# Optimization experiments

Hardware: AMD Instinct MI355X
Metric: run time of the kernel (lower is better)

The kernel has to match this reference:

```python
import jax, jax.numpy as jnp
import numpy as np


def setup_inputs() -> dict:
    key = jax.random.key(0)
    k1, k2 = jax.random.split(key)
    # [1, D, H, W, C] cubic feature volume
    image_features = jax.random.normal(k1, (1, 64, 64, 64, 64), dtype=jnp.float32)
    # [1, N, 3] vertex coords in the original 128^3 volume, in [0, 128)
    graph_features = jax.random.uniform(k2, (1, 200000, 3), dtype=jnp.float32) * 128.0
    return {"image_features": image_features, "graph_features": graph_features}


def reference(image_features, graph_features):
    img = image_features[0]                      # [D, H, W, C]
    H = img.shape[0]
    factor = jnp.float32(128.0 / H)
    x = graph_features[..., -3] / factor         # [B, N]
    y = graph_features[..., -2] / factor
    z = graph_features[..., -1] / factor
    hm1 = jnp.float32(H - 1)
    x1 = jnp.floor(x); x2 = jnp.minimum(jnp.ceil(x), hm1)
    y1 = jnp.floor(y); y2 = jnp.minimum(jnp.ceil(y), hm1)
    z1 = jnp.floor(z); z2 = jnp.minimum(jnp.ceil(z), hm1)

    def gather(ix, iy, iz):
        # [B, N] index arrays -> [B, N, C] gathered features
        return img[ix.astype(jnp.int32), iy.astype(jnp.int32), iz.astype(jnp.int32)]

    wx = (x - x1)[..., None]; wx2 = (x2 - x)[..., None]
    wy = (y - y1)[..., None]; wy2 = (y2 - y)[..., None]
    wz = (z - z1)[..., None]; wz2 = (z2 - z)[..., None]

    # z = z1 plane
    q11 = gather(x1, y1, z1); q21 = gather(x2, y1, z1)
    q12 = gather(x1, y2, z1); q22 = gather(x2, y2, z1)
    lerp_y1 = (q22 * wx + q12 * wx2) * wy + (q21 * wx + q11 * wx2) * wy2

    # z = z2 plane
    q11 = gather(x1, y1, z2); q21 = gather(x2, y1, z2)
    q12 = gather(x1, y2, z2); q22 = gather(x2, y2, z2)
    lerp_y2 = (q22 * wx + q12 * wx2) * wy + (q21 * wx + q11 * wx2) * wy2

    return lerp_y2 * wz + lerp_y1 * wz2          # [B, N, C]
```

## Files before the change

### kernel.cpp

```cpp
#include <hip/hip_runtime.h>


__device__ __forceinline__ float4 f4mul(float4 a, float s) {
    return make_float4(a.x * s, a.y * s, a.z * s, a.w * s);
}
__device__ __forceinline__ float4 f4fma(float4 a, float s, float4 acc) {
    return make_float4(fmaf(a.x, s, acc.x), fmaf(a.y, s, acc.y),
                       fmaf(a.z, s, acc.z), fmaf(a.w, s, acc.w));
}

__global__ __launch_bounds__(256) void trilerp_kernel(
    const float* __restrict__ img, const float* __restrict__ coords,
    float* __restrict__ out, int n_points)
{
    int tid = blockIdx.x * 256 + threadIdx.x;
    int p = tid >> 4;
    if (p >= n_points) return;
    int cvec = tid & 15;

    float x = coords[3 * p + 0] * 0.5f;
    float y = coords[3 * p + 1] * 0.5f;
    float z = coords[3 * p + 2] * 0.5f;

    float fx1 = floorf(x), fx2 = fminf(ceilf(x), 63.0f);
    float fy1 = floorf(y), fy2 = fminf(ceilf(y), 63.0f);
    float fz1 = floorf(z), fz2 = fminf(ceilf(z), 63.0f);

    float wx = x - fx1, wxc = fx2 - x;
    float wy = y - fy1, wyc = fy2 - y;
    float wz = z - fz1, wzc = fz2 - z;

    int ix1 = (int)fx1, ix2 = (int)fx2;
    int iy1 = (int)fy1, iy2 = (int)fy2;
    int iz1 = (int)fz1, iz2 = (int)fz2;

    const float4* __restrict__ imgv = (const float4*)img;
    int bx1 = ix1 << 12, bx2 = ix2 << 12;
    int by1 = iy1 << 6,  by2 = iy2 << 6;

    float4 q11 = imgv[((bx1 + by1 + iz1) << 4) + cvec];
    float4 q21 = imgv[((bx2 + by1 + iz1) << 4) + cvec];
    float4 q12 = imgv[((bx1 + by2 + iz1) << 4) + cvec];
    float4 q22 = imgv[((bx2 + by2 + iz1) << 4) + cvec];
    float4 ly1 = f4fma(f4fma(q22, wx, f4mul(q12, wxc)), wy,
                       f4mul(f4fma(q21, wx, f4mul(q11, wxc)), wyc));

    q11 = imgv[((bx1 + by1 + iz2) << 4) + cvec];
    q21 = imgv[((bx2 + by1 + iz2) << 4) + cvec];
    q12 = imgv[((bx1 + by2 + iz2) << 4) + cvec];
    q22 = imgv[((bx2 + by2 + iz2) << 4) + cvec];
    float4 ly2 = f4fma(f4fma(q22, wx, f4mul(q12, wxc)), wy,
                       f4mul(f4fma(q21, wx, f4mul(q11, wxc)), wyc));

    float4 res = f4fma(ly2, wz, f4mul(ly1, wzc));
    ((float4*)out)[(p << 4) + cvec] = res;
}

extern "C" void kernel_launch(void* const* d_in, const int* in_sizes, int n_in,
                              void* d_out, int out_size, void* d_ws, size_t ws_size,
                              hipStream_t stream) {
    const float* img    = (const float*)d_in[0];
    const float* coords = (const float*)d_in[1];
    float* out = (float*)d_out;
    int n_points = in_sizes[1] / 3;

    int threads = n_points * 16;
    int grid = (threads + 255) / 256;
    trilerp_kernel<<<grid, 256, 0, stream>>>(img, coords, out, n_points);
}
```

Before: 147.7 us.

## Sort points by Morton bin before trilinear gather for cache locality

Adds a counting sort of the points into 32768 Morton-ordered spatial bins (histogram, single-block scan, atomic scatter into a workspace buffer). The gather kernel then walks points in sorted order, so nearby points share cached voxel neighborhoods, and it remaps block IDs so each XCD handles a contiguous range of bins. The aim is to cut the random 16 MB volume gathers that miss in L2. The cost is four extra launches plus a memset, a serial single-block scan, and scattered output writes indexed by the original point ID.

```diff
diff --git a/kernel.cpp b/kernel.cpp
--- a/kernel.cpp
+++ b/kernel.cpp
@@ -1,5 +1,9 @@
 #include <hip/hip_runtime.h>
 
+
+#define NBINS 32768
+#define SCAN_THREADS 1024
+#define BINS_PER_THREAD 32
 
 __device__ __forceinline__ float4 f4mul(float4 a, float s) {
     return make_float4(a.x * s, a.y * s, a.z * s, a.w * s);
@@ -7,6 +11,118 @@
 __device__ __forceinline__ float4 f4fma(float4 a, float s, float4 acc) {
     return make_float4(fmaf(a.x, s, acc.x), fmaf(a.y, s, acc.y),
                        fmaf(a.z, s, acc.z), fmaf(a.w, s, acc.w));
+}
+
+__device__ __forceinline__ unsigned part1by2(unsigned x) {
+    x &= 0x3FF;
+    x = (x | (x << 16)) & 0x030000FF;
+    x = (x | (x << 8))  & 0x0300F00F;
+    x = (x | (x << 4))  & 0x030C30C3;
+    x = (x | (x << 2))  & 0x09249249;
+    return x;
+}
+
+__device__ __forceinline__ int bin_of(float xs, float ys, float zs) {
+    unsigned bx = ((unsigned)(int)floorf(xs)) >> 1;
+    unsigned by = ((unsigned)(int)floorf(ys)) >> 1;
+    unsigned bz = ((unsigned)(int)floorf(zs)) >> 1;
+    return (int)(part1by2(bx) | (part1by2(by) << 1) | (part1by2(bz) << 2));
+}
+
+__global__ __launch_bounds__(256) void hist_kernel(
+    const float* __restrict__ coords, int* __restrict__ bins, int n)
+{
+    int p = blockIdx.x * 256 + threadIdx.x;
+    if (p >= n) return;
+    float xs = coords[3 * p + 0] * 0.5f;
+    float ys = coords[3 * p + 1] * 0.5f;
+    float zs = coords[3 * p + 2] * 0.5f;
+    atomicAdd(&bins[bin_of(xs, ys, zs)], 1);
+}
+
+__global__ __launch_bounds__(SCAN_THREADS) void scan_kernel(int* __restrict__ bins)
+{
+    __shared__ int sums[SCAN_THREADS];
+    int t = threadIdx.x;
+    int base = t * BINS_PER_THREAD;
+    int local[BINS_PER_THREAD];
+    int s = 0;
+    #pragma unroll
+    for (int i = 0; i < BINS_PER_THREAD; i++) local[i] = bins[base + i];
+    #pragma unroll
+    for (int i = 0; i < BINS_PER_THREAD; i++) { int v = local[i]; local[i] = s; s += v; }
+    sums[t] = s;
+    __syncthreads();
+    for (int off = 1; off < SCAN_THREADS; off <<= 1) {
+        int v = (t >= off) ? sums[t - off] : 0;
+        __syncthreads();
+        sums[t] += v;
+        __syncthreads();
+    }
+    int prefix = (t == 0) ? 0 : sums[t - 1];
+    #pragma unroll
+    for (int i = 0; i < BINS_PER_THREAD; i++) bins[base + i] = local[i] + prefix;
+}
+
+__global__ __launch_bounds__(256) void scatter_kernel(
+    const float* __restrict__ coords, int* __restrict__ offs,
+    float4* __restrict__ coordsS, int n)
+{
+    int p = blockIdx.x * 256 + threadIdx.x;
+    if (p >= n) return;
+    float xs = coords[3 * p + 0] * 0.5f;
+    float ys = coords[3 * p + 1] * 0.5f;
+    float zs = coords[3 * p + 2] * 0.5f;
+    int r = atomicAdd(&offs[bin_of(xs, ys, zs)], 1);
+    coordsS[r] = make_float4(xs, ys, zs, __int_as_float(p));
+}
+
+__global__ __launch_bounds__(256) void trilerp_sorted_kernel(
+    const float* __restrict__ img, const float4* __restrict__ coordsS,
+    float* __restrict__ out, int n_points, int per_xcd)
+{
+    int b = (blockIdx.x & 7) * per_xcd + (blockIdx.x >> 3);
+    int tid = b * 256 + threadIdx.x;
+    int sp = tid >> 4;
+    if (sp >= n_points) return;
+    int cvec = tid & 15;
+
+    float4 cs = coordsS[sp];
+    float x = cs.x, y = cs.y, z = cs.z;
+    int p = __float_as_int(cs.w);
+
+    float fx1 = floorf(x), fx2 = fminf(ceilf(x), 63.0f);
+    float fy1 = floorf(y), fy2 = fminf(ceilf(y), 63.0f);
+    float fz1 = floorf(z), fz2 = fminf(ceilf(z), 63.0f);
+
+    float wx = x - fx1, wxc = fx2 - x;
+    float wy = y - fy1, wyc = fy2 - y;
+    float wz = z - fz1, wzc = fz2 - z;
+
+    int ix1 = (int)fx1, ix2 = (int)fx2;
+    int iy1 = (int)fy1, iy2 = (int)fy2;
+    int iz1 = (int)fz1, iz2 = (int)fz2;
+
+    const float4* __restrict__ imgv = (const float4*)img;
+    int bx1 = ix1 << 12, bx2 = ix2 << 12;
+    int by1 = iy1 << 6,  by2 = iy2 << 6;
+
+    float4 q11 = imgv[((bx1 + by1 + iz1) << 4) + cvec];
+    float4 q21 = imgv[((bx2 + by1 + iz1) << 4) + cvec];
+    float4 q12 = imgv[((bx1 + by2 + iz1) << 4) + cvec];
+    float4 q22 = imgv[((bx2 + by2 + iz1) << 4) + cvec];
+    float4 ly1 = f4fma(f4fma(q22, wx, f4mul(q12, wxc)), wy,
+                       f4mul(f4fma(q21, wx, f4mul(q11, wxc)), wyc));
+
+    q11 = imgv[((bx1 + by1 + iz2) << 4) + cvec];
+    q21 = imgv[((bx2 + by1 + iz2) << 4) + cvec];
+    q12 = imgv[((bx1 + by2 + iz2) << 4) + cvec];
+    q22 = imgv[((bx2 + by2 + iz2) << 4) + cvec];
+    float4 ly2 = f4fma(f4fma(q22, wx, f4mul(q12, wxc)), wy,
+                       f4mul(f4fma(q21, wx, f4mul(q11, wxc)), wyc));
+
+    float4 res = f4fma(ly2, wz, f4mul(ly1, wzc));
+    ((float4*)out)[(p << 4) + cvec] = res;
 }
 
 __global__ __launch_bounds__(256) void trilerp_kernel(
@@ -62,9 +178,31 @@
     const float* img    = (const float*)d_in[0];
     const float* coords = (const float*)d_in[1];
     float* out = (float*)d_out;
-    int n_points = in_sizes[1] / 3;
-
-    int threads = n_points * 16;
-    int grid = (threads + 255) / 256;
-    trilerp_kernel<<<grid, 256, 0, stream>>>(img, coords, out, n_points);
-}
+    int n = in_sizes[1] / 3;
+
+    size_t bins_bytes   = (size_t)NBINS * sizeof(int);
+    size_t coordsS_off  = bins_bytes;
+    size_t need = coordsS_off + (size_t)n * sizeof(float4);
+
+    if (ws_size >= need) {
+        int* bins       = (int*)d_ws;
+        float4* coordsS = (float4*)((char*)d_ws + coordsS_off);
+
+        hipMemsetAsync(bins, 0, bins_bytes, stream);
+
+        int pgrid = (n + 255) / 256;
+        hist_kernel<<<pgrid, 256, 0, stream>>>(coords, bins, n);
+        scan_kernel<<<1, SCAN_THREADS, 0, stream>>>(bins);
+        scatter_kernel<<<pgrid, 256, 0, stream>>>(coords, bins, coordsS, n);
+
+        int threads = n * 16;
+        int nb = (threads + 255) / 256;
+        int nb_pad = (nb + 7) & ~7;
+        int per_xcd = nb_pad >> 3;
+        trilerp_sorted_kernel<<<nb_pad, 256, 0, stream>>>(img, coordsS, out, n, per_xcd);
+    } else {
+        int threads = n * 16;
+        int grid = (threads + 255) / 256;
+        trilerp_kernel<<<grid, 256, 0, stream>>>(img, coords, out, n);
+    }
+}
```

After: 155.1 us. 5.0% more time.

## Bin points into spatial buckets and trilerp from LDS-staged volume tiles

Applied to the files above, without the earlier changes.

A new scatter kernel bins every query point into one of 4096 buckets, each covering a 4x4x4 voxel region, using atomic slot counters. Points past the per-bucket capacity go to an overflow list. A gather kernel then loads a 5x5x5 halo tile of the feature volume into LDS once per bucket and interpolates all of that bucket's points from shared memory. This is meant to replace eight scattered global reads per point with mostly coalesced tile loads. It costs a memset, an extra kernel launch, atomics and roughly 8 MB of workspace, and points beyond the overflow capacity would be silently dropped.

```diff
diff --git a/kernel.cpp b/kernel.cpp
--- a/kernel.cpp
+++ b/kernel.cpp
@@ -1,5 +1,12 @@
 #include <hip/hip_runtime.h>
 
+
+#define NBUCK   4096
+#define CAP     128
+#define OVCAP   8192
+#define TILE_F4 2000
+
+typedef float __attribute__((ext_vector_type(4))) fx4;
 
 __device__ __forceinline__ float4 f4mul(float4 a, float s) {
     return make_float4(a.x * s, a.y * s, a.z * s, a.w * s);
@@ -7,6 +14,131 @@
 __device__ __forceinline__ float4 f4fma(float4 a, float s, float4 acc) {
     return make_float4(fmaf(a.x, s, acc.x), fmaf(a.y, s, acc.y),
                        fmaf(a.z, s, acc.z), fmaf(a.w, s, acc.w));
+}
+
+__global__ __launch_bounds__(256) void scatter_kernel(
+    const float* __restrict__ coords, int* __restrict__ counts,
+    float4* __restrict__ buckets, float4* __restrict__ overflow, int n)
+{
+    int p = blockIdx.x * 256 + threadIdx.x;
+    if (p >= n) return;
+    float xs = coords[3 * p + 0] * 0.5f;
+    float ys = coords[3 * p + 1] * 0.5f;
+    float zs = coords[3 * p + 2] * 0.5f;
+    int vx = (int)floorf(xs), vy = (int)floorf(ys), vz = (int)floorf(zs);
+    int bucket = ((vx >> 2) << 8) | ((vy >> 2) << 4) | (vz >> 2);
+    int slot = atomicAdd(&counts[bucket], 1);
+    float4 v = make_float4(xs, ys, zs, __int_as_float(p));
+    if (slot < CAP) {
+        buckets[bucket * CAP + slot] = v;
+    } else {
+        int o = atomicAdd(&counts[NBUCK], 1);
+        if (o < OVCAP) overflow[o] = v;
+    }
+}
+
+__global__ __launch_bounds__(256) void gather_kernel(
+    const float* __restrict__ img, const int* __restrict__ counts,
+    const float4* __restrict__ buckets, const float4* __restrict__ overflow,
+    float* __restrict__ out)
+{
+    const float4* __restrict__ imgv = (const float4*)img;
+    int cvec = threadIdx.x & 15;
+    int grp  = threadIdx.x >> 4;
+
+    if (blockIdx.x < NBUCK) {
+        __shared__ float4 tile[TILE_F4];
+        int bucket = (blockIdx.x & 7) * 512 + (blockIdx.x >> 3);
+        int bx0 = (bucket >> 8) << 2;
+        int by0 = ((bucket >> 4) & 15) << 2;
+        int bz0 = (bucket & 15) << 2;
+
+        for (int f = threadIdx.x; f < TILE_F4; f += 256) {
+            int tv = f >> 4, c = f & 15;
+            int lz = tv % 5, t2 = tv / 5;
+            int ly = t2 % 5, lx = t2 / 5;
+            int gx = min(bx0 + lx, 63), gy = min(by0 + ly, 63), gz = min(bz0 + lz, 63);
+            tile[f] = imgv[(((((gx << 6) + gy) << 6) + gz) << 4) + c];
+        }
+        int cnt = min(counts[bucket], CAP);
+        __syncthreads();
+
+        for (int i = grp; i < cnt; i += 16) {
+            float4 cs = buckets[bucket * CAP + i];
+            float x = cs.x, y = cs.y, z = cs.z;
+            int p = __float_as_int(cs.w);
+
+            float fx1 = floorf(x), fx2 = fminf(ceilf(x), 63.0f);
+            float fy1 = floorf(y), fy2 = fminf(ceilf(y), 63.0f);
+            float fz1 = floorf(z), fz2 = fminf(ceilf(z), 63.0f);
+
+            int lx1 = (int)fx1 - bx0, lx2 = (int)fx2 - bx0;
+            int ly1 = (int)fy1 - by0, ly2 = (int)fy2 - by0;
+            int lz1 = (int)fz1 - bz0, lz2 = (int)fz2 - bz0;
+            int ax1 = lx1 * 25, ax2 = lx2 * 25;
+            int ay1 = ly1 * 5,  ay2 = ly2 * 5;
+
+            float4 q111 = tile[((ax1 + ay1 + lz1) << 4) + cvec];
+            float4 q211 = tile[((ax2 + ay1 + lz1) << 4) + cvec];
+            float4 q121 = tile[((ax1 + ay2 + lz1) << 4) + cvec];
+            float4 q221 = tile[((ax2 + ay2 + lz1) << 4) + cvec];
+            float4 q112 = tile[((ax1 + ay1 + lz2) << 4) + cvec];
+            float4 q212 = tile[((ax2 + ay1 + lz2) << 4) + cvec];
+            float4 q122 = tile[((ax1 + ay2 + lz2) << 4) + cvec];
+            float4 q222 = tile[((ax2 + ay2 + lz2) << 4) + cvec];
+
+            float wx = x - fx1, wxc = fx2 - x;
+            float wy = y - fy1, wyc = fy2 - y;
+            float wz = z - fz1, wzc = fz2 - z;
+
+            float4 ly1v = f4fma(f4fma(q221, wx, f4mul(q121, wxc)), wy,
+                                f4mul(f4fma(q211, wx, f4mul(q111, wxc)), wyc));
+            float4 ly2v = f4fma(f4fma(q222, wx, f4mul(q122, wxc)), wy,
+                                f4mul(f4fma(q212, wx, f4mul(q112, wxc)), wyc));
+            float4 res = f4fma(ly2v, wz, f4mul(ly1v, wzc));
+
+            fx4 r; r.x = res.x; r.y = res.y; r.z = res.z; r.w = res.w;
+            __builtin_nontemporal_store(r, (fx4*)out + (p << 4) + cvec);
+        }
+    } else {
+        int ob = blockIdx.x - NBUCK;
+        int cnt = min(counts[NBUCK], OVCAP);
+        for (int i = (ob << 4) + grp; i < cnt; i += 32 * 16) {
+            float4 cs = overflow[i];
+            float x = cs.x, y = cs.y, z = cs.z;
+            int p = __float_as_int(cs.w);
+
+            float fx1 = floorf(x), fx2 = fminf(ceilf(x), 63.0f);
+            float fy1 = floorf(y), fy2 = fminf(ceilf(y), 63.0f);
+            float fz1 = floorf(z), fz2 = fminf(ceilf(z), 63.0f);
+
+            int bx1 = ((int)fx1) << 12, bx2 = ((int)fx2) << 12;
+            int by1 = ((int)fy1) << 6,  by2 = ((int)fy2) << 6;
+            int iz1 = (int)fz1, iz2 = (int)fz2;
+
+            float4 q111 = imgv[((bx1 + by1 + iz1) << 4) + cvec];
+            float4 q211 = imgv[((bx2 + by1 + iz1) << 4) + cvec];
+            float4 q121 = imgv[((bx1 + by2 + iz1) << 4) + cvec];
+            float4 q221 = imgv[((bx2 + by2 + iz1) << 4) + cvec];
+            float4 q112 = imgv[((bx1 + by1 + iz2) << 4) + cvec];
+            float4 q212 = imgv[((bx2 + by1 + iz2) << 4) + cvec];
+            float4 q122 = imgv[((bx1 + by2 + iz2) << 4) + cvec];
+            float4 q222 = imgv[((bx2 + by2 + iz2) << 4) + cvec];
+
+            float wx = x - fx1, wxc = fx2 - x;
+            float wy = y - fy1, wyc = fy2 - y;
+            float wz = z - fz1, wzc = fz2 - z;
+
+            float4 ly1v = f4fma(f4fma(q221, wx, f4mul(q121, wxc)), wy,
+                                f4mul(f4fma(q211, wx, f4mul(q111, wxc)), wyc));
+            float4 ly2v = f4fma(f4fma(q222, wx, f4mul(q122, wxc)), wy,
+                                f4mul(f4fma(q212, wx, f4mul(q112, wxc)), wyc));
+            float4 res = f4fma(ly2v, wz, f4mul(ly1v, wzc));
+
+            fx4 r; r.x = res.x; r.y = res.y; r.z = res.z; r.w = res.w;
+            __builtin_nontemporal_store(r, (fx4*)out + (p << 4) + cvec);
+        }
+    }
 }
 
 __global__ __launch_bounds__(256) void trilerp_kernel(
@@ -30,13 +162,10 @@
     float wy = y - fy1, wyc = fy2 - y;
     float wz = z - fz1, wzc = fz2 - z;
 
-    int ix1 = (int)fx1, ix2 = (int)fx2;
-    int iy1 = (int)fy1, iy2 = (int)fy2;
+    const float4* __restrict__ imgv = (const float4*)img;
+    int bx1 = ((int)fx1) << 12, bx2 = ((int)fx2) << 12;
+    int by1 = ((int)fy1) << 6,  by2 = ((int)fy2) << 6;
     int iz1 = (int)fz1, iz2 = (int)fz2;
-
-    const float4* __restrict__ imgv = (const float4*)img;
-    int bx1 = ix1 << 12, bx2 = ix2 << 12;
-    int by1 = iy1 << 6,  by2 = iy2 << 6;
 
     float4 q11 = imgv[((bx1 + by1 + iz1) << 4) + cvec];
     float4 q21 = imgv[((bx2 + by1 + iz1) << 4) + cvec];
@@ -62,9 +191,26 @@
     const float* img    = (const float*)d_in[0];
     const float* coords = (const float*)d_in[1];
     float* out = (float*)d_out;
-    int n_points = in_sizes[1] / 3;
-
-    int threads = n_points * 16;
-    int grid = (threads + 255) / 256;
-    trilerp_kernel<<<grid, 256, 0, stream>>>(img, coords, out, n_points);
-}
+    int n = in_sizes[1] / 3;
+
+    size_t counts_bytes = 32768;
+    size_t buckets_off  = counts_bytes;
+    size_t buckets_bytes = (size_t)NBUCK * CAP * sizeof(float4);
+    size_t overflow_off = buckets_off + buckets_bytes;
+    size_t need = overflow_off + (size_t)OVCAP * sizeof(float4);
+
+    if (ws_size >= need) {
+        int*    counts   = (int*)d_ws;
+        float4* buckets  = (float4*)((char*)d_ws + buckets_off);
+        float4* overflow = (float4*)((char*)d_ws + overflow_off);
+
+        hipMemsetAsync(counts, 0, (NBUCK + 1) * sizeof(int), stream);
+        int pgrid = (n + 255) / 256;
+        scatter_kernel<<<pgrid, 256, 0, stream>>>(coords, counts, buckets, overflow, n);
+        gather_kernel<<<NBUCK + 32, 256, 0, stream>>>(img, counts, buckets, overflow, out);
+    } else {
+        int threads = n * 16;
+        int grid = (threads + 255) / 256;
+        trilerp_kernel<<<grid, 256, 0, stream>>>(img, coords, out, n);
+    }
+}
```

Measured after the change: 150.6 us. Within noise of the previous version (+1.9%).
